# Performance work log

Hardware: AMD Instinct MI355X
Metric: run time of the kernel (lower is better)

## Reference

```python
import jax, jax.numpy as jnp
import numpy as np

K = 0.1
GAMMA = 1.0


def setup_inputs() -> dict:
    key = jax.random.key(0)
    k1, k2, k3, k4, k5 = jax.random.split(key, 5)
    N, M, D = 16384, 2048, 128
    # Points must lie inside the Poincare ball (0 < norm < 1) for acos/asin validity.
    x = jax.random.normal(k1, (N, D), dtype=jnp.float32)
    x = x / jnp.linalg.norm(x, axis=1, keepdims=True)
    x = x * jax.random.uniform(k2, (N, 1), minval=0.3, maxval=0.9, dtype=jnp.float32)
    p = jax.random.normal(k3, (M, D), dtype=jnp.float32)
    p = p / jnp.linalg.norm(p, axis=1, keepdims=True)
    p = p * jax.random.uniform(k4, (M, 1), minval=0.3, maxval=0.9, dtype=jnp.float32)
    labels = jax.random.randint(k5, (N,), 0, M)
    return {"x": x, "p": p, "labels": labels}


def reference(x, p, labels):
    N = x.shape[0]
    dot = x @ p.T                                   # [N, M], replaces NxMxD broadcast
    nx2 = jnp.sum(x * x, axis=1, keepdims=True)     # [N, 1] = ||x||^2
    np2 = jnp.sum(p * p, axis=1)                    # [M]    = ||p||^2
    np_norm = jnp.sqrt(np2)                         # [M]

    num = dot * (1.0 + np2) - np2 * (1.0 + nx2)     # [N, M]
    # Faithful to original: sum of squared pairwise distances over the BATCH axis (dim=0)
    # sum_i ||x_i - p_j||^2 = sum_i||x_i||^2 + N*||p_j||^2 - 2*(sum_i x_i)@p_j
    sum_sq_dist = jnp.sum(nx2) + N * np2 - 2.0 * (jnp.sum(x, axis=0) @ p.T)  # [M]
    den = np_norm * jnp.sqrt(sum_sq_dist) * jnp.sqrt(1.0 + np2 * nx2 - 2.0 * dot)  # [N, M]
    angle = jnp.arccos(num / den)                   # [N, M]

    psi = jnp.arcsin(K * (1.0 - np2) / np_norm)     # [M], broadcast over rows
    angles = jnp.maximum(0.0, angle - psi)          # [N, M]

    rows = jnp.arange(N)
    positive = angles[rows, labels]                 # [N]
    neg = jnp.maximum(0.0, GAMMA - angles)          # [N, M]
    negative = jnp.sum(neg, axis=1) - neg[rows, labels]  # exclude label column
    return jnp.mean(positive + negative)
```

## Files before the change

### kernel.cpp

```cpp
#include <hip/hip_runtime.h>
#include <math.h>

#define KCONST 0.1f
#define GAMMA_C 1.0f
#define D_DIM 128

typedef __attribute__((ext_vector_type(8))) short bf16x8;
typedef __attribute__((ext_vector_type(4))) float f32x4;

#define ASYNC_COPY16(gsrc, ldst)                                                  \
  __builtin_amdgcn_global_load_lds(                                               \
      (const __attribute__((address_space(1))) void*)(gsrc),                      \
      (__attribute__((address_space(3))) void*)(ldst), 16, 0, 0)

__device__ __forceinline__ unsigned short f2bf(float f) {
  unsigned int u = __float_as_uint(f);
  u += 0x7fffu + ((u >> 16) & 1u);
  return (unsigned short)(u >> 16);
}

__global__ void prep_x(const float* __restrict__ x, unsigned short* __restrict__ xb,
                       float* __restrict__ nx2, float* __restrict__ pSumX,
                       float* __restrict__ pS2, int N) {
  const int tid = threadIdx.x;
  const int l = tid & 63, w = tid >> 6;
  const int l16 = l & 15, sub = l >> 4;
  const int waveId = blockIdx.x * 4 + w;
  const float4* x4 = (const float4*)x;
  ushort4* xb4 = (ushort4*)xb;
  float4 c0 = {0.f, 0.f, 0.f, 0.f}, c1 = {0.f, 0.f, 0.f, 0.f};
  float s2 = 0.f;
#pragma unroll
  for (int it = 0; it < 4; ++it) {
    int row = (waveId + it * 1024) * 4 + sub;
    float4 v0 = x4[row * 32 + l16];
    float4 v1 = x4[row * 32 + 16 + l16];
    c0.x += v0.x; c0.y += v0.y; c0.z += v0.z; c0.w += v0.w;
    c1.x += v1.x; c1.y += v1.y; c1.z += v1.z; c1.w += v1.w;
    ushort4 b0, b1;
    b0.x = f2bf(v0.x); b0.y = f2bf(v0.y); b0.z = f2bf(v0.z); b0.w = f2bf(v0.w);
    b1.x = f2bf(v1.x); b1.y = f2bf(v1.y); b1.z = f2bf(v1.z); b1.w = f2bf(v1.w);
    xb4[row * 32 + l16] = b0;
    xb4[row * 32 + 16 + l16] = b1;
    float sq = v0.x * v0.x;
    sq = fmaf(v0.y, v0.y, sq); sq = fmaf(v0.z, v0.z, sq); sq = fmaf(v0.w, v0.w, sq);
    sq = fmaf(v1.x, v1.x, sq); sq = fmaf(v1.y, v1.y, sq);
    sq = fmaf(v1.z, v1.z, sq); sq = fmaf(v1.w, v1.w, sq);
    sq += __shfl_down(sq, 8); sq += __shfl_down(sq, 4);
    sq += __shfl_down(sq, 2); sq += __shfl_down(sq, 1);
    if (l16 == 0) {
      nx2[row] = sq;
      s2 += sq;
    }
  }
  s2 += __shfl_down(s2, 16);
  s2 += __shfl_down(s2, 32);
  __shared__ float cs[128];
  __shared__ float s2w[4];
  if (tid < 128) cs[tid] = 0.f;
  if (l == 0) s2w[w] = s2;
  __syncthreads();
  atomicAdd(&cs[l16 * 4 + 0], c0.x); atomicAdd(&cs[l16 * 4 + 1], c0.y);
  atomicAdd(&cs[l16 * 4 + 2], c0.z); atomicAdd(&cs[l16 * 4 + 3], c0.w);
  atomicAdd(&cs[64 + l16 * 4 + 0], c1.x); atomicAdd(&cs[64 + l16 * 4 + 1], c1.y);
  atomicAdd(&cs[64 + l16 * 4 + 2], c1.z); atomicAdd(&cs[64 + l16 * 4 + 3], c1.w);
  __syncthreads();
  if (tid < 128) pSumX[blockIdx.x * 128 + tid] = cs[tid];
  if (tid == 0) pS2[blockIdx.x] = s2w[0] + s2w[1] + s2w[2] + s2w[3];
}

__global__ void merge_sums(const float* __restrict__ pSumX, const float* __restrict__ pS2,
                           float* __restrict__ sum_x, float* __restrict__ sum_nx2) {
  __shared__ float seg[8][128];
  __shared__ float s2w[4];
  const int t = threadIdx.x;
  const int col = t & 127;
  const int sg = t >> 7;
  float s = 0.f;
#pragma unroll
  for (int b = 0; b < 32; ++b) s += pSumX[(sg * 32 + b) * 128 + col];
  seg[sg][col] = s;
  float s2 = (t < 256) ? pS2[t] : 0.f;
  if (t < 256) {
#pragma unroll
    for (int off = 32; off; off >>= 1) s2 += __shfl_down(s2, off);
    if ((t & 63) == 0) s2w[t >> 6] = s2;
  }
  __syncthreads();
  if (t < 128) {
    float r = 0.f;
#pragma unroll
    for (int k = 0; k < 8; ++k) r += seg[k][col];
    sum_x[t] = r;
  }
  if (t == 0) sum_nx2[0] = s2w[0] + s2w[1] + s2w[2] + s2w[3];
}

__global__ void prep_p(const float* __restrict__ p, unsigned short* __restrict__ pb,
                       const float* __restrict__ sum_x, const float* __restrict__ sum_nx2,
                       float4* __restrict__ colc, float* __restrict__ psiA,
                       int M, int N) {
  const int lane = threadIdx.x & 63;
  const int wave = threadIdx.x >> 6;
  const int j = blockIdx.x * 4 + wave;
  if (j >= M) return;
  const float2* p2 = (const float2*)p;
  ushort2* pb2 = (ushort2*)pb;
  float2 v = p2[j * 64 + lane];
  ushort2 b;
  b.x = f2bf(v.x);
  b.y = f2bf(v.y);
  pb2[j * 64 + lane] = b;
  float np2 = fmaf(v.x, v.x, v.y * v.y);
  float sd = fmaf(v.x, sum_x[2 * lane], v.y * sum_x[2 * lane + 1]);
#pragma unroll
  for (int off = 32; off; off >>= 1) {
    np2 += __shfl_down(np2, off);
    sd += __shfl_down(sd, off);
  }
  if (lane == 0) {
    float ssd = *sum_nx2 + (float)N * np2 - 2.f * sd;
    float npn = sqrtf(np2);
    float cfi = 1.f / (npn * sqrtf(ssd));
    float4 cc;
    cc.x = (1.f + np2) * cfi;
    cc.y = np2 * cfi;
    cc.z = np2;
    cc.w = np2 / (1.f + np2);
    colc[j] = cc;
    psiA[j] = asinf(KCONST * (1.f - np2) / npn);
  }
}

__global__ __launch_bounds__(256, 2) void pair_mfma(
    const unsigned short* __restrict__ xb, const unsigned short* __restrict__ pb,
    const int* __restrict__ labels, const float* __restrict__ nx2,
    const float4* __restrict__ colc, const float* __restrict__ psiA,
    float* __restrict__ partials) {
  __shared__ float4 xs4[2048];
  __shared__ float4 ps4[2048];
  __shared__ float nxs[128];
  __shared__ int lbs[128];
  __shared__ float wred[4];

  const int tid = threadIdx.x;
  const int l = tid & 63;
  const int w = tid >> 6;
  const int row0 = blockIdx.y * 128;
  const int col0 = blockIdx.x * 128;
  const float4* xg = (const float4*)(xb + (size_t)row0 * D_DIM);
  const float4* pg = (const float4*)(pb + (size_t)col0 * D_DIM);

#pragma unroll
  for (int ci = w; ci < 32; ci += 4) {
    int qi = ci * 64 + l;
    int r = qi >> 4, ql = qi & 15;
    int srcq = r * 16 + (ql ^ (r & 15));
    ASYNC_COPY16(xg + srcq, xs4 + ci * 64);
    ASYNC_COPY16(pg + srcq, ps4 + ci * 64);
  }
  if (tid < 128) {
    nxs[tid] = 1.f + nx2[row0 + tid];
    lbs[tid] = labels[row0 + tid];
  }
  __syncthreads();

  const int m = tid & 15;
  const int q = (tid >> 4) & 3;
  const int wr = (w & 1) * 64;
  const int wc = (w >> 1) * 64;

  f32x4 acc[4][4];
#pragma unroll
  for (int r = 0; r < 4; ++r)
#pragma unroll
    for (int c = 0; c < 4; ++c) acc[r][c] = (f32x4)(0.f);

#pragma unroll
  for (int s = 0; s < 4; ++s) {
    const int qphys = (s * 4 + q) ^ m;
    bf16x8 a[4], b[4];
#pragma unroll
    for (int r = 0; r < 4; ++r) {
      a[r] = __builtin_bit_cast(bf16x8, xs4[(wr + r * 16 + m) * 16 + qphys]);
      b[r] = __builtin_bit_cast(bf16x8, ps4[(wc + r * 16 + m) * 16 + qphys]);
    }
#pragma unroll
    for (int r = 0; r < 4; ++r)
#pragma unroll
      for (int c = 0; c < 4; ++c)
        acc[r][c] = __builtin_amdgcn_mfma_f32_16x16x32_bf16(a[r], b[c], acc[r][c], 0, 0, 0);
  }

  float4 cc[4];
  int cols[4];
#pragma unroll
  for (int c = 0; c < 4; ++c) {
    cols[c] = col0 + wc + c * 16 + m;
    cc[c] = colc[cols[c]];
  }

  float ssum = 0.f;
#pragma unroll
  for (int r = 0; r < 4; ++r) {
    const f32x4 rnp4 = __builtin_bit_cast(f32x4, *(const float4*)&nxs[wr + r * 16 + q * 4]);
    const int4 lb4 = *(const int4*)&lbs[wr + r * 16 + q * 4];
#pragma unroll
    for (int c = 0; c < 4; ++c) {
      const f32x4 dv = acc[r][c];
      const float Tc = cc[c].w;
      float e0 = fmaf(-Tc, rnp4[0], dv[0]);
      float e1 = fmaf(-Tc, rnp4[1], dv[1]);
      float e2 = fmaf(-Tc, rnp4[2], dv[2]);
      float e3 = fmaf(-Tc, rnp4[3], dv[3]);
      float hm = fmaxf(fmaxf(e0, e1), fmaxf(e2, e3));
      bool h = (hm > 0.f) | (cols[c] == lb4.x) | (cols[c] == lb4.y) |
               (cols[c] == lb4.z) | (cols[c] == lb4.w);
      if (__builtin_expect(h, 0)) {
        const float psi = psiA[cols[c]];
        const float C1 = 1.f + psi;
        const float omnp2 = 1.f - cc[c].z;
#pragma unroll
        for (int g = 0; g < 4; ++g) {
          float rnp = rnp4[g];
          float dot = dv[g];
          int lb = (g == 0) ? lb4.x : (g == 1) ? lb4.y : (g == 2) ? lb4.z : lb4.w;
          float den2 = fmaf(cc[c].z, rnp, omnp2) - 2.f * dot;
          float nump = fmaf(dot, cc[c].x, -cc[c].y * rnp);
          float u = nump * __builtin_amdgcn_rsqf(den2);
          u = __builtin_amdgcn_fmed3f(u, -1.f, 1.f);
          float ax = fabsf(u);
          float rt = __builtin_amdgcn_sqrtf(1.f - ax);
          float poly = fmaf(fmaf(fmaf(-0.0187293f, ax, 0.0742610f), ax, -0.2121144f),
                            ax, 1.5707288f);
          float ac = rt * poly;
          ac = (u >= 0.f) ? ac : 3.14159265358979f - ac;
          float neg = __builtin_amdgcn_fmed3f(C1 - ac, 0.f, 1.f);
          float pos = fmaxf(0.f, ac - psi);
          ssum += (cols[c] == lb) ? pos : neg;
        }
      }
    }
  }

#pragma unroll
  for (int off = 32; off; off >>= 1) ssum += __shfl_down(ssum, off);
  if (l == 0) wred[w] = ssum;
  __syncthreads();
  if (tid == 0)
    partials[blockIdx.y * gridDim.x + blockIdx.x] = wred[0] + wred[1] + wred[2] + wred[3];
}

__global__ void finalize(const float* __restrict__ partials, float* __restrict__ out,
                         int n, float invN) {
  float s = 0.f;
  for (int i = threadIdx.x; i < n; i += 256) s += partials[i];
#pragma unroll
  for (int off = 32; off; off >>= 1) s += __shfl_down(s, off);
  __shared__ float wred[4];
  if ((threadIdx.x & 63) == 0) wred[threadIdx.x >> 6] = s;
  __syncthreads();
  if (threadIdx.x == 0) out[0] = (wred[0] + wred[1] + wred[2] + wred[3]) * invN;
}

extern "C" void kernel_launch(void* const* d_in, const int* in_sizes, int n_in,
                              void* d_out, int out_size, void* d_ws, size_t ws_size,
                              hipStream_t stream) {
  const float* x = (const float*)d_in[0];
  const float* p = (const float*)d_in[1];
  const int* labels = (const int*)d_in[2];
  float* out = (float*)d_out;
  const int N = in_sizes[2];
  const int M = in_sizes[1] / D_DIM;

  float* ws = (float*)d_ws;
  float* nx2 = ws;
  float4* colc = (float4*)(ws + N);
  float* psiA = ws + N + 4 * M;
  unsigned short* xb = (unsigned short*)(ws + N + 5 * M);
  unsigned short* pb = (unsigned short*)(ws + N + 5 * M + 64 * N);
  float* pSumX = ws + N + 5 * M + 64 * N + 64 * M;
  float* pS2 = pSumX + 256 * 128;
  float* sum_x = pS2 + 256;
  float* sum_nx2 = sum_x + 128;
  float* partials = sum_nx2 + 4;

  prep_x<<<256, 256, 0, stream>>>(x, xb, nx2, pSumX, pS2, N);
  merge_sums<<<1, 1024, 0, stream>>>(pSumX, pS2, sum_x, sum_nx2);
  prep_p<<<M / 4, 256, 0, stream>>>(p, pb, sum_x, sum_nx2, colc, psiA, M, N);

  dim3 grid(M / 128, N / 128);
  pair_mfma<<<grid, 256, 0, stream>>>(xb, pb, labels, nx2, colc, psiA, partials);

  finalize<<<1, 256, 0, stream>>>(partials, out, 2048, 1.0f / (float)N);
}
```

Before: 96.57 us.

## Load MFMA operands directly from global memory instead of staging in LDS

```diff
diff --git a/kernel.cpp b/kernel.cpp
--- a/kernel.cpp
+++ b/kernel.cpp
@@ -7,11 +7,6 @@
 
 typedef __attribute__((ext_vector_type(8))) short bf16x8;
 typedef __attribute__((ext_vector_type(4))) float f32x4;
-
-#define ASYNC_COPY16(gsrc, ldst)                                                  \
-  __builtin_amdgcn_global_load_lds(                                               \
-      (const __attribute__((address_space(1))) void*)(gsrc),                      \
-      (__attribute__((address_space(3))) void*)(ldst), 16, 0, 0)
 
 __device__ __forceinline__ unsigned short f2bf(float f) {
   unsigned int u = __float_as_uint(f);
@@ -20,7 +15,7 @@
 }
 
 __global__ void prep_x(const float* __restrict__ x, unsigned short* __restrict__ xb,
-                       float* __restrict__ nx2, float* __restrict__ pSumX,
+                       float* __restrict__ nx2p, float* __restrict__ pSumX,
                        float* __restrict__ pS2, int N) {
   const int tid = threadIdx.x;
   const int l = tid & 63, w = tid >> 6;
@@ -49,7 +44,7 @@
     sq += __shfl_down(sq, 8); sq += __shfl_down(sq, 4);
     sq += __shfl_down(sq, 2); sq += __shfl_down(sq, 1);
     if (l16 == 0) {
-      nx2[row] = sq;
+      nx2p[row] = 1.f + sq;
       s2 += sq;
     }
   }
@@ -132,44 +127,25 @@
   }
 }
 
-__global__ __launch_bounds__(256, 2) void pair_mfma(
+__global__ __launch_bounds__(256, 4) void pair_mfma(
     const unsigned short* __restrict__ xb, const unsigned short* __restrict__ pb,
-    const int* __restrict__ labels, const float* __restrict__ nx2,
+    const int* __restrict__ labels, const float* __restrict__ nx2p,
     const float4* __restrict__ colc, const float* __restrict__ psiA,
     float* __restrict__ partials) {
-  __shared__ float4 xs4[2048];
-  __shared__ float4 ps4[2048];
-  __shared__ float nxs[128];
-  __shared__ int lbs[128];
   __shared__ float wred[4];
-
   const int tid = threadIdx.x;
   const int l = tid & 63;
   const int w = tid >> 6;
   const int row0 = blockIdx.y * 128;
   const int col0 = blockIdx.x * 128;
-  const float4* xg = (const float4*)(xb + (size_t)row0 * D_DIM);
-  const float4* pg = (const float4*)(pb + (size_t)col0 * D_DIM);
-
-#pragma unroll
-  for (int ci = w; ci < 32; ci += 4) {
-    int qi = ci * 64 + l;
-    int r = qi >> 4, ql = qi & 15;
-    int srcq = r * 16 + (ql ^ (r & 15));
-    ASYNC_COPY16(xg + srcq, xs4 + ci * 64);
-    ASYNC_COPY16(pg + srcq, ps4 + ci * 64);
-  }
-  if (tid < 128) {
-    nxs[tid] = 1.f + nx2[row0 + tid];
-    lbs[tid] = labels[row0 + tid];
-  }
-  __syncthreads();
-
   const int m = tid & 15;
   const int q = (tid >> 4) & 3;
   const int wr = (w & 1) * 64;
   const int wc = (w >> 1) * 64;
 
+  const float4* xg = (const float4*)(xb + (size_t)(row0 + wr) * D_DIM);
+  const float4* pg = (const float4*)(pb + (size_t)(col0 + wc) * D_DIM);
+
   f32x4 acc[4][4];
 #pragma unroll
   for (int r = 0; r < 4; ++r)
@@ -178,13 +154,13 @@
 
 #pragma unroll
   for (int s = 0; s < 4; ++s) {
-    const int qphys = (s * 4 + q) ^ m;
     bf16x8 a[4], b[4];
 #pragma unroll
-    for (int r = 0; r < 4; ++r) {
-      a[r] = __builtin_bit_cast(bf16x8, xs4[(wr + r * 16 + m) * 16 + qphys]);
-      b[r] = __builtin_bit_cast(bf16x8, ps4[(wc + r * 16 + m) * 16 + qphys]);
-    }
+    for (int r = 0; r < 4; ++r)
+      a[r] = __builtin_bit_cast(bf16x8, xg[(r * 16 + m) * 16 + s * 4 + q]);
+#pragma unroll
+    for (int c = 0; c < 4; ++c)
+      b[c] = __builtin_bit_cast(bf16x8, pg[(c * 16 + m) * 16 + s * 4 + q]);
 #pragma unroll
     for (int r = 0; r < 4; ++r)
 #pragma unroll
@@ -199,12 +175,19 @@
     cols[c] = col0 + wc + c * 16 + m;
     cc[c] = colc[cols[c]];
   }
+  float4 rnp4v[4];
+  int4 lb4v[4];
+#pragma unroll
+  for (int r = 0; r < 4; ++r) {
+    rnp4v[r] = *(const float4*)&nx2p[row0 + wr + r * 16 + q * 4];
+    lb4v[r] = *(const int4*)&labels[row0 + wr + r * 16 + q * 4];
+  }
 
   float ssum = 0.f;
 #pragma unroll
   for (int r = 0; r < 4; ++r) {
-    const f32x4 rnp4 = __builtin_bit_cast(f32x4, *(const float4*)&nxs[wr + r * 16 + q * 4]);
-    const int4 lb4 = *(const int4*)&lbs[wr + r * 16 + q * 4];
+    const f32x4 rnp4 = __builtin_bit_cast(f32x4, rnp4v[r]);
+    const int4 lb4 = lb4v[r];
 #pragma unroll
     for (int c = 0; c < 4; ++c) {
       const f32x4 dv = acc[r][c];
@@ -274,7 +257,7 @@
   const int M = in_sizes[1] / D_DIM;
 
   float* ws = (float*)d_ws;
-  float* nx2 = ws;
+  float* nx2p = ws;
   float4* colc = (float4*)(ws + N);
   float* psiA = ws + N + 4 * M;
   unsigned short* xb = (unsigned short*)(ws + N + 5 * M);
@@ -285,12 +268,12 @@
   float* sum_nx2 = sum_x + 128;
   float* partials = sum_nx2 + 4;
 
-  prep_x<<<256, 256, 0, stream>>>(x, xb, nx2, pSumX, pS2, N);
+  prep_x<<<256, 256, 0, stream>>>(x, xb, nx2p, pSumX, pS2, N);
   merge_sums<<<1, 1024, 0, stream>>>(pSumX, pS2, sum_x, sum_nx2);
   prep_p<<<M / 4, 256, 0, stream>>>(p, pb, sum_x, sum_nx2, colc, psiA, M, N);
 
   dim3 grid(M / 128, N / 128);
-  pair_mfma<<<grid, 256, 0, stream>>>(xb, pb, labels, nx2, colc, psiA, partials);
+  pair_mfma<<<grid, 256, 0, stream>>>(xb, pb, labels, nx2p, colc, psiA, partials);
 
   finalize<<<1, 256, 0, stream>>>(partials, out, 2048, 1.0f / (float)N);
 }
```

Result: slower. 113.9 us (+17.9%).
